# Optimization experiments

Measured on AMD Instinct MI355X. Metric: run time of the kernel, lower is better.

Reference implementation:

```python
import jax, jax.numpy as jnp
import numpy as np

B_, C0, H_, W_ = 2, 64, 128, 128
NB = 4          # number of VSS blocks (depths=[4])
K = 4           # scan directions
DI = 128        # d_inner = 2.0 * 64
N = 16          # ssm_d_state
R = 4           # dt_rank = ceil(64/16)


def setup_inputs() -> dict:
    key = jax.random.key(0)
    ks = jax.random.split(key, 16)
    rn = lambda k, shape, s: jax.random.normal(k, shape, jnp.float32) * s
    inp = {}
    inp["inp_img"] = jax.random.normal(ks[0], (B_, 1, H_, W_), jnp.float32)
    inp["x"] = jax.random.normal(ks[1], (B_, C0, H_, W_), jnp.float32)
    inp["y"] = jax.random.normal(ks[2], (B_, C0, H_, W_), jnp.float32)
    inp["reduce_w"] = rn(ks[3], (64, 128, 1, 1), 0.05)
    inp["patch_w"] = rn(ks[4], (64, 64, 1, 1), 0.05)
    inp["patch_g"] = jnp.ones((64,)); inp["patch_b"] = jnp.zeros((64,))
    inp["ln1_g"] = jnp.ones((NB, 64)); inp["ln1_b"] = jnp.zeros((NB, 64))
    inp["in_proj_w"] = rn(ks[5], (NB, 2 * DI, 64), 0.05)
    inp["conv_w"] = rn(ks[6], (NB, DI, 1, 3, 3), 0.1)   # depthwise 3x3
    inp["conv_b"] = jnp.zeros((NB, DI))
    inp["x_proj_w"] = rn(ks[7], (NB, K, R + 2 * N, DI), 0.05)
    inp["dt_proj_w"] = rn(ks[8], (NB, K, DI, R), 0.1)
    inp["dt_proj_b"] = rn(ks[9], (NB, K, DI), 0.1)
    A = jnp.tile(jnp.arange(1, N + 1, dtype=jnp.float32)[None, :], (K * DI, 1))
    inp["A_logs"] = jnp.tile(jnp.log(A)[None], (NB, 1, 1))
    inp["Ds_p"] = jnp.ones((NB, K * DI))
    inp["out_norm_g"] = jnp.ones((NB, DI)); inp["out_norm_b"] = jnp.zeros((NB, DI))
    inp["out_proj_w"] = rn(ks[10], (NB, 64, DI), 0.05)
    inp["ln2_g"] = jnp.ones((NB, 64)); inp["ln2_b"] = jnp.zeros((NB, 64))
    inp["fc1_w"] = rn(ks[11], (NB, 256, 64), 0.05); inp["fc1_b"] = jnp.zeros((NB, 256))
    inp["fc2_w"] = rn(ks[12], (NB, 64, 256), 0.05); inp["fc2_b"] = jnp.zeros((NB, 64))
    inp["out1_w"] = rn(ks[13], (32, 64, 3, 3), 0.05)
    inp["out2_w"] = rn(ks[14], (1, 32, 3, 3), 0.05)
    return inp


def conv2d(t, w, pad=0, groups=1):
    return jax.lax.conv_general_dilated(
        t, w, (1, 1), [(pad, pad), (pad, pad)],
        dimension_numbers=("NCHW", "OIHW", "NCHW"), feature_group_count=groups)


def ln(t, g, b):
    mu = t.mean(-1, keepdims=True)
    v = t.var(-1, keepdims=True)
    return (t - mu) / jnp.sqrt(v + 1e-5) * g + b


def ssm_scan(u, delta, A, Bs, Cs):
    # u, delta: (B,K,D,L); A: (K,D,N); Bs, Cs: (B,K,N,L)
    Bn = u.shape[0]
    ut = jnp.moveaxis(u, -1, 0)      # (L,B,K,D)
    dt = jnp.moveaxis(delta, -1, 0)
    Bt = jnp.moveaxis(Bs, -1, 0)     # (L,B,K,N)
    Ct = jnp.moveaxis(Cs, -1, 0)
    h0 = jnp.zeros((Bn, K, DI, N), u.dtype)
    def step(h, inp):
        u_, d_, b_, c_ = inp
        h = jnp.exp(d_[..., None] * A) * h + (d_ * u_)[..., None] * b_[:, :, None, :]
        return h, jnp.sum(h * c_[:, :, None, :], -1)
    _, ys = jax.lax.scan(step, h0, (ut, dt, Bt, Ct))
    return jnp.moveaxis(ys, 0, -1)   # (B,K,D,L)


def vss_block(t, i, ln1_g, ln1_b, in_proj_w, conv_w, conv_b, x_proj_w,
              dt_proj_w, dt_proj_b, A_logs, Ds_p, out_norm_g, out_norm_b,
              out_proj_w, ln2_g, ln2_b, fc1_w, fc1_b, fc2_w, fc2_b):
    # t: (B,H,W,64)
    h = ln(t, ln1_g[i], ln1_b[i])
    xz = jnp.einsum("bhwc,oc->bhwo", h, in_proj_w[i])     # (B,H,W,2*DI)
    xp, zp = jnp.split(xz, 2, axis=-1)
    xc = jnp.transpose(xp, (0, 3, 1, 2))                    # (B,DI,H,W)
    xc = conv2d(xc, conv_w[i], pad=1, groups=DI) + conv_b[i][None, :, None, None]
    xc = jax.nn.silu(xc)
    Bn, D, H, W = xc.shape
    L = H * W
    x_hw = xc.reshape(Bn, D, L)
    x_wh = jnp.transpose(xc, (0, 1, 3, 2)).reshape(Bn, D, L)
    xs = jnp.stack([x_hw, x_wh, jnp.flip(x_hw, -1), jnp.flip(x_wh, -1)], 1)  # (B,K,D,L)
    x_dbl = jnp.einsum("bkdl,kcd->bkcl", xs, x_proj_w[i])
    dts, Bs, Cs = jnp.split(x_dbl, [R, R + N], axis=2)
    dts = jnp.einsum("bkrl,kdr->bkdl", dts, dt_proj_w[i])
    delta = jax.nn.softplus(dts + dt_proj_b[i][None, :, :, None])
    A = -jnp.exp(A_logs[i]).reshape(K, D, N)
    ys = ssm_scan(xs, delta, A, Bs, Cs)
    ys = ys + Ds_p[i].reshape(K, D)[None, :, :, None] * xs
    # cross-merge
    ym = ys[:, 0] + jnp.flip(ys[:, 2], -1)
    ywh = ys[:, 1] + jnp.flip(ys[:, 3], -1)
    ym = ym + jnp.transpose(ywh.reshape(Bn, D, W, H), (0, 1, 3, 2)).reshape(Bn, D, L)
    yo = jnp.transpose(ym.reshape(Bn, D, H, W), (0, 2, 3, 1))  # (B,H,W,DI)
    yo = ln(yo, out_norm_g[i], out_norm_b[i])
    yo = yo * jax.nn.silu(zp)
    t = t + jnp.einsum("bhwd,od->bhwo", yo, out_proj_w[i])
    m = ln(t, ln2_g[i], ln2_b[i])
    m = jax.nn.gelu(jnp.einsum("bhwc,oc->bhwo", m, fc1_w[i]) + fc1_b[i], approximate=False)
    m = jnp.einsum("bhwc,oc->bhwo", m, fc2_w[i]) + fc2_b[i]
    return t + m


def reference(inp_img, x, y, reduce_w, patch_w, patch_g, patch_b, ln1_g, ln1_b,
              in_proj_w, conv_w, conv_b, x_proj_w, dt_proj_w, dt_proj_b, A_logs,
              Ds_p, out_norm_g, out_norm_b, out_proj_w, ln2_g, ln2_b, fc1_w,
              fc1_b, fc2_w, fc2_b, out1_w, out2_w):
    f = conv2d(jnp.concatenate([x, y], 1), reduce_w)          # (B,64,H,W)
    t = jnp.transpose(conv2d(f, patch_w), (0, 2, 3, 1))        # (B,H,W,64)
    t = ln(t, patch_g, patch_b)
    for i in range(NB):
        t = vss_block(t, i, ln1_g, ln1_b, in_proj_w, conv_w, conv_b, x_proj_w,
                      dt_proj_w, dt_proj_b, A_logs, Ds_p, out_norm_g, out_norm_b,
                      out_proj_w, ln2_g, ln2_b, fc1_w, fc1_b, fc2_w, fc2_b)
    z = jnp.transpose(t, (0, 3, 1, 2))                         # (B,64,H,W)
    o = conv2d(z, out1_w, pad=1)
    o = jnp.where(o >= 0, o, 0.01 * o)                         # LeakyReLU
    o = conv2d(o, out2_w, pad=1) + inp_img
    return jax.nn.sigmoid(o), f
```

## Files before the change

kernel.cpp:

```cpp
#include <hip/hip_runtime.h>
#include <math.h>

#define B_ 2
#define H_ 128
#define W_ 128
#define L_ (H_*W_)
#define DI 128
#define NK 4
#define NST 16
#define NBLK 4
#define C36 36

__device__ __forceinline__ int scan_src(int k, int l){
  if (k == 0)      return l;
  else if (k == 1) return ((l & 127) << 7) | (l >> 7);
  else if (k == 2) return L_-1-l;
  else { int m = L_-1-l; return ((m & 127) << 7) | (m >> 7); }
}

template<int NCHT>
__device__ __forceinline__ void scan_decode(int g, int& b, int& k, int& c){
  int xcd = g & 7, s = g >> 3;
  int m = s & 1, qh = s >> 1;
  int q = qh*8 + xcd;
  b = q / (2*NCHT);
  int rc = (q / NCHT) & 1;
  int cc = q % NCHT;
  k = rc ? (m ? 3 : 1) : (m ? 2 : 0);
  c = m ? (NCHT-1-cc) : cc;
}

__global__ void k_repack(const float* __restrict__ inw, const float* __restrict__ f1w,
                         const float* __restrict__ f2w, const float* __restrict__ opw,
                         const float* __restrict__ redw, const float* __restrict__ patw,
                         const float* __restrict__ o1w, const float* __restrict__ o2w,
                         const float* __restrict__ xpjw, float* __restrict__ wr){
  int idx = blockIdx.x*256 + threadIdx.x;
  if (idx >= 358688) return;
  float v;
  if (idx < 65536){
    int i = idx >> 14, r = idx & 16383; int k = r >> 8, o = r & 255;
    v = inw[(size_t)(i*256 + o)*64 + k];
  } else if (idx < 131072){
    int j = idx - 65536; int i = j >> 14, r = j & 16383; int k = r >> 8, o = r & 255;
    v = f1w[(size_t)(i*256 + o)*64 + k];
  } else if (idx < 196608){
    int j = idx - 131072; int i = j >> 14, r = j & 16383; int k = r >> 6, o = r & 63;
    v = f2w[(size_t)(i*64 + o)*256 + k];
  } else if (idx < 229376){
    int j = idx - 196608; int i = j >> 13, r = j & 8191; int k = r >> 6, o = r & 63;
    v = opw[(size_t)(i*64 + o)*128 + k];
  } else if (idx < 237568){
    int j = idx - 229376; int k = j >> 6, o = j & 63;
    v = redw[o*128 + k];
  } else if (idx < 241664){
    int j = idx - 237568; int k = j >> 6, o = j & 63;
    v = patw[o*64 + k];
  } else if (idx < 260096){
    int j = idx - 241664; int tap = j >> 11, r = j & 2047; int k = r >> 5, o = r & 31;
    v = o1w[(size_t)(o*64 + k)*9 + tap];
  } else if (idx < 260384){
    int j = idx - 260096; int tap = j >> 5, c = j & 31;
    v = o2w[c*9 + tap];
  } else {
    int j = idx - 260384;
    int grp = j / 1536, r3 = j % 1536;
    int d = r3 / 12, jj = r3 % 12;
    int cg = grp & 3; int ik = grp >> 2;
    v = (jj < 9) ? xpjw[((size_t)(ik*36) + cg*9 + jj)*128 + d] : 0.f;
  }
  wr[idx] = v;
}

__global__ __launch_bounds__(256) void k_reduce(
    const float* __restrict__ x, const float* __restrict__ y,
    const float* __restrict__ w, float* __restrict__ f){
  __shared__ float Xs[128*68];
  int tid = threadIdx.x;
  int blk = blockIdx.x; int b = blk >> 8; int l0 = (blk & 255)*64;
  const float* xb = x + (size_t)b*64*L_ + l0;
  const float* yb = y + (size_t)b*64*L_ + l0;
  #pragma unroll
  for (int rep = 0; rep < 32; ++rep){
    int idx = rep*256 + tid;
    int k = idx >> 6, p = idx & 63;
    float v = (k < 64) ? xb[(size_t)k*L_ + p] : yb[(size_t)(k-64)*L_ + p];
    Xs[k*68 + p] = v;
  }
  __syncthreads();
  int p0 = (tid & 15)*4, o0 = (tid >> 4)*4;
  float acc[4][4] = {};
  #pragma unroll 2
  for (int k = 0; k < 128; ++k){
    float4 xa = *(const float4*)&Xs[k*68 + p0];
    float4 wa = *(const float4*)&w[k*64 + o0];
    float xv[4] = {xa.x,xa.y,xa.z,xa.w};
    float wv[4] = {wa.x,wa.y,wa.z,wa.w};
    #pragma unroll
    for (int a = 0; a < 4; ++a)
      #pragma unroll
      for (int o = 0; o < 4; ++o) acc[a][o] += xv[a]*wv[o];
  }
  #pragma unroll
  for (int o = 0; o < 4; ++o){
    float* dst = f + (size_t)(b*64 + o0 + o)*L_ + l0 + p0;
    *(float4*)dst = make_float4(acc[0][o],acc[1][o],acc[2][o],acc[3][o]);
  }
}

__global__ __launch_bounds__(256) void k_patch_ln(
    const float* __restrict__ f, const float* __restrict__ w,
    const float* __restrict__ pg, const float* __restrict__ pb,
    float* __restrict__ t){
  __shared__ float Xs[64*68];
  __shared__ float Os[64*65];
  __shared__ float stat[128];
  int tid = threadIdx.x;
  int blk = blockIdx.x; int b = blk >> 8; int l0 = (blk & 255)*64;
  const float* fb = f + (size_t)b*64*L_ + l0;
  #pragma unroll
  for (int rep = 0; rep < 16; ++rep){
    int idx = rep*256 + tid;
    int k = idx >> 6, p = idx & 63;
    Xs[k*68 + p] = fb[(size_t)k*L_ + p];
  }
  __syncthreads();
  int p0 = (tid & 15)*4, o0 = (tid >> 4)*4;
  float acc[4][4] = {};
  #pragma unroll 2
  for (int k = 0; k < 64; ++k){
    float4 xa = *(const float4*)&Xs[k*68 + p0];
    float4 wa = *(const float4*)&w[k*64 + o0];
    float xv[4] = {xa.x,xa.y,xa.z,xa.w};
    float wv[4] = {wa.x,wa.y,wa.z,wa.w};
    #pragma unroll
    for (int a = 0; a < 4; ++a)
      #pragma unroll
      for (int o = 0; o < 4; ++o) acc[a][o] += xv[a]*wv[o];
  }
  #pragma unroll
  for (int a = 0; a < 4; ++a)
    #pragma unroll
    for (int o = 0; o < 4; ++o)
      Os[(p0+a)*65 + o0+o] = acc[a][o];
  __syncthreads();
  if (tid < 64){
    float s = 0.f, s2 = 0.f;
    #pragma unroll
    for (int c = 0; c < 64; ++c){ float v = Os[tid*65+c]; s += v; s2 += v*v; }
    float mu = s*(1.f/64), var = s2*(1.f/64) - mu*mu;
    stat[tid*2] = mu; stat[tid*2+1] = rsqrtf(var + 1e-5f);
  }
  __syncthreads();
  #pragma unroll
  for (int rep = 0; rep < 16; ++rep){
    int idx = rep*256 + tid;
    int p = idx >> 6, c = idx & 63;
    float mu = stat[p*2], rstd = stat[p*2+1];
    t[(size_t)blk*64*64 + idx] = (Os[p*65+c]-mu)*rstd*pg[c] + pb[c];
  }
}

__global__ __launch_bounds__(256) void k_ln_inproj(
    const float* __restrict__ t, const float* __restrict__ g,
    const float* __restrict__ bta, const float* __restrict__ w,
    float* __restrict__ xp, float* __restrict__ zt){
  __shared__ float raw[64*65];
  __shared__ float Xs[64*68];
  __shared__ float scr[512];
  __shared__ float stat[128];
  int tid = threadIdx.x;
  int pix0 = blockIdx.x*64;
  const float* tb = t + (size_t)pix0*64;
  #pragma unroll
  for (int rep = 0; rep < 16; ++rep){
    int idx = rep*256 + tid;
    int p = idx >> 6, c = idx & 63;
    raw[p*65 + c] = tb[idx];
  }
  __syncthreads();
  int p = tid & 63, q = tid >> 6;
  {
    float s = 0.f, s2 = 0.f;
    #pragma unroll
    for (int i = 0; i < 16; ++i){ float v = raw[p*65 + q*16 + i]; s += v; s2 += v*v; }
    scr[p*8 + q*2] = s; scr[p*8 + q*2 + 1] = s2;
  }
  __syncthreads();
  if (tid < 64){
    float s = 0.f, s2 = 0.f;
    #pragma unroll
    for (int j = 0; j < 4; ++j){ s += scr[tid*8 + j*2]; s2 += scr[tid*8 + j*2 + 1]; }
    float mu = s*(1.f/64), var = s2*(1.f/64) - mu*mu;
    stat[tid] = mu; stat[64+tid] = rsqrtf(var + 1e-5f);
  }
  __syncthreads();
  {
    float mu = stat[p], rstd = stat[64+p];
    #pragma unroll
    for (int i = 0; i < 16; ++i){
      int c = q*16 + i;
      Xs[c*68 + p] = (raw[p*65+c] - mu)*rstd*g[c] + bta[c];
    }
  }
  __syncthreads();
  int p0 = (tid & 7)*8, o0 = (tid >> 3)*8;
  float acc[8][8] = {};
  #pragma unroll 2
  for (int k = 0; k < 64; ++k){
    float4 xa = *(const float4*)&Xs[k*68 + p0];
    float4 xb = *(const float4*)&Xs[k*68 + p0 + 4];
    float4 wa = *(const float4*)&w[k*256 + o0];
    float4 wb = *(const float4*)&w[k*256 + o0 + 4];
    float xv[8] = {xa.x,xa.y,xa.z,xa.w,xb.x,xb.y,xb.z,xb.w};
    float wv[8] = {wa.x,wa.y,wa.z,wa.w,wb.x,wb.y,wb.z,wb.w};
    #pragma unroll
    for (int a = 0; a < 8; ++a)
      #pragma unroll
      for (int o = 0; o < 8; ++o) acc[a][o] += xv[a]*wv[o];
  }
  if (o0 < 128){
    float* base = xp + (size_t)pix0*128 + o0;
    #pragma unroll
    for (int a = 0; a < 8; ++a){
      float* dst = base + (size_t)(p0+a)*128;
      *(float4*)dst     = make_float4(acc[a][0],acc[a][1],acc[a][2],acc[a][3]);
      *(float4*)(dst+4) = make_float4(acc[a][4],acc[a][5],acc[a][6],acc[a][7]);
    }
  } else {
    int oz = o0 - 128;
    float* dstz = zt + (size_t)blockIdx.x*8192;
    #pragma unroll
    for (int o = 0; o < 8; ++o){
      *(float4*)&dstz[(oz+o)*64 + p0]     = make_float4(acc[0][o],acc[1][o],acc[2][o],acc[3][o]);
      *(float4*)&dstz[(oz+o)*64 + p0 + 4] = make_float4(acc[4][o],acc[5][o],acc[6][o],acc[7][o]);
    }
  }
}

__global__ __launch_bounds__(256) void k_dwconv(
    const float* __restrict__ xp, const float* __restrict__ cw,
    const float* __restrict__ cb, float* __restrict__ xc){
  int idx = blockIdx.x*256 + threadIdx.x;
  int d = idx & 127; int tt = idx >> 7;
  int w = tt & 127; tt >>= 7;
  int h0 = (tt & 31)*4; int b = tt >> 5;
  float wt[9];
  #pragma unroll
  for (int q = 0; q < 9; ++q) wt[q] = cw[d*9+q];
  float cbv = cb[d];
  float acc[4] = {cbv, cbv, cbv, cbv};
  const float* base = xp + (size_t)(b*L_)*128 + d;
  #pragma unroll
  for (int r = 0; r < 6; ++r){
    int rr = h0 - 1 + r;
    if ((unsigned)rr >= 128u) continue;
    const float* rowp = base + (size_t)(rr*128 + w)*128;
    float mid   = rowp[0];
    float left  = (w > 0)   ? rowp[-128] : 0.f;
    float right = (w < 127) ? rowp[128]  : 0.f;
    #pragma unroll
    for (int i = 0; i < 4; ++i){
      int kh = rr - (h0 + i) + 1;
      if (0 <= kh && kh <= 2)
        acc[i] += left*wt[kh*3] + mid*wt[kh*3+1] + right*wt[kh*3+2];
    }
  }
  #pragma unroll
  for (int i = 0; i < 4; ++i){
    float a = acc[i];
    xc[((size_t)(b*L_ + (h0+i)*128 + w))*128 + d] = a/(1.f + __expf(-a));
  }
}

__global__ __launch_bounds__(256) void k_xproj(
    const float* __restrict__ xc, const float* __restrict__ wxp,
    float* __restrict__ xdbl){
  int lt = blockIdx.x & 255; int bk = blockIdx.x >> 8;
  int b = bk >> 2, k = bk & 3;
  int l0 = lt*64;
  __shared__ float Ws[4*128*12];
  __shared__ float Xs[64*129];
  int tid = threadIdx.x;
  const float* wsrc = wxp + (size_t)k*6144;
  for (int j = tid; j < 6144; j += 256) Ws[j] = wsrc[j];
  for (int j = tid; j < 64*128; j += 256){
    int lr = j >> 7, d = j & 127;
    Xs[lr*129 + d] = xc[((size_t)(b*L_ + l0 + lr))*128 + d];
  }
  __syncthreads();
  int lx = tid & 63, cg = tid >> 6;
  float acc[9];
  #pragma unroll
  for (int j = 0; j < 9; ++j) acc[j] = 0.f;
  const float* xrow = Xs + lx*129;
  const float* wbase = Ws + cg*128*12;
  #pragma unroll 4
  for (int d = 0; d < 128; ++d){
    float xv = xrow[d];
    const float* wd = wbase + d*12;
    float4 wa = *(const float4*)wd;
    float4 wb = *(const float4*)(wd+4);
    float w8 = wd[8];
    acc[0]+=xv*wa.x; acc[1]+=xv*wa.y; acc[2]+=xv*wa.z; acc[3]+=xv*wa.w;
    acc[4]+=xv*wb.x; acc[5]+=xv*wb.y; acc[6]+=xv*wb.z; acc[7]+=xv*wb.w;
    acc[8]+=xv*w8;
  }
  float* out = xdbl + ((size_t)bk*L_ + l0 + lx)*C36 + cg*9;
  #pragma unroll
  for (int j = 0; j < 9; ++j) out[j] = acc[j];
}

template<int PASS, int NCHT, int LCT>
__global__ __launch_bounds__(128, 2) void k_scan_chunk(
    const float* __restrict__ xc, const float* __restrict__ xdbl,
    const float* __restrict__ dtw, const float* __restrict__ dtb,
    const float* __restrict__ ds,
    float* __restrict__ chS, float* __restrict__ chH,
    float* __restrict__ ym){
  __shared__ float rowS[LCT*36];
  int b, k, c;
  scan_decode<NCHT>(blockIdx.x, b, k, c);
  int bk = b*4 + k;
  int blk = bk*NCHT + c;
  int tid = threadIdx.x;
  int d = tid;
  const float* xdb = xdbl + (size_t)bk*L_*C36;
  const int F4 = (PASS == 0) ? 5 : 9;
  for (int idx = tid; idx < LCT*F4; idx += 128){
    int r = idx / F4, f4 = idx - r*F4;
    int src = scan_src(k, c*LCT + r);
    *(float4*)&rowS[r*36 + f4*4] = *(const float4*)(xdb + (size_t)src*C36 + f4*4);
  }
  float4 wv4 = *(const float4*)(dtw + (size_t)(k*128+d)*4);
  float w0 = wv4.x, w1 = wv4.y, w2 = wv4.z, w3 = wv4.w;
  float bb = dtb[k*128+d];
  float Dsv = ds[k*128+d];
  float h[16];
  float S = 0.f;
  size_t chbase = ((size_t)blk*128 + d)*16;
  if (PASS == 0){
    #pragma unroll
    for (int n = 0; n < 16; ++n) h[n] = 0.f;
  } else {
    #pragma unroll
    for (int qq = 0; qq < 4; ++qq){
      float4 v = *(const float4*)(chH + chbase + qq*4);
      h[qq*4+0]=v.x; h[qq*4+1]=v.y; h[qq*4+2]=v.z; h[qq*4+3]=v.w;
    }
  }
  int sbase = scan_src(k, c*LCT);
  int sstep = (k == 0) ? 1 : (k == 1) ? 128 : (k == 2) ? -1 : -128;
  ptrdiff_t stepOff = (ptrdiff_t)sstep*128;
  const float* up = xc + (size_t)b*L_*128 + (size_t)sbase*128 + d;
  float* yp = ym + (size_t)b*L_*128 + (size_t)sbase*128 + d;
  __syncthreads();
  float u = *up;
  #pragma unroll 2
  for (int j = 0; j < LCT; ++j){
    up += stepOff;
    float u_nxt = *up;
    const float* r = rowS + j*36;
    float4 dtv = *(const float4*)r;
    float xdt = bb + dtv.x*w0 + dtv.y*w1 + dtv.z*w2 + dtv.w*w3;
    float ex = __expf(xdt);
    float delta = (xdt > 20.f) ? xdt : __logf(1.f + ex);
    float e1 = __builtin_amdgcn_rcpf(1.f + ex);
    float e2 = e1*e1, e3 = e2*e1, e4 = e2*e2;
    float e8 = e4*e4, e12 = e8*e4;
    float mm[16];
    mm[0]=e1;      mm[1]=e2;      mm[2]=e3;      mm[3]=e4;
    mm[4]=e4*e1;   mm[5]=e4*e2;   mm[6]=e4*e3;   mm[7]=e8;
    mm[8]=e8*e1;   mm[9]=e8*e2;   mm[10]=e8*e3;  mm[11]=e8*e4;
    mm[12]=e12*e1; mm[13]=e12*e2; mm[14]=e12*e3; mm[15]=e12*e4;
    float du = delta * u;
    if (PASS == 0){
      S += delta;
      #pragma unroll
      for (int qq = 0; qq < 4; ++qq){
        float4 Bq = *(const float4*)(r + 4 + qq*4);
        h[qq*4+0] = mm[qq*4+0]*h[qq*4+0] + du*Bq.x;
        h[qq*4+1] = mm[qq*4+1]*h[qq*4+1] + du*Bq.y;
        h[qq*4+2] = mm[qq*4+2]*h[qq*4+2] + du*Bq.z;
        h[qq*4+3] = mm[qq*4+3]*h[qq*4+3] + du*Bq.w;
      }
    } else {
      float y = Dsv * u;
      #pragma unroll
      for (int qq = 0; qq < 4; ++qq){
        float4 Bq = *(const float4*)(r + 4 + qq*4);
        float4 Cq = *(const float4*)(r + 20 + qq*4);
        h[qq*4+0] = mm[qq*4+0]*h[qq*4+0] + du*Bq.x;  y += h[qq*4+0]*Cq.x;
        h[qq*4+1] = mm[qq*4+1]*h[qq*4+1] + du*Bq.y;  y += h[qq*4+1]*Cq.y;
        h[qq*4+2] = mm[qq*4+2]*h[qq*4+2] + du*Bq.z;  y += h[qq*4+2]*Cq.z;
        h[qq*4+3] = mm[qq*4+3]*h[qq*4+3] + du*Bq.w;  y += h[qq*4+3]*Cq.w;
      }
      atomicAdd(yp, y);
      yp += stepOff;
    }
    u = u_nxt;
  }
  if (PASS == 0){
    #pragma unroll
    for (int qq = 0; qq < 4; ++qq)
      *(float4*)(chH + chbase + qq*4) =
        make_float4(h[qq*4+0],h[qq*4+1],h[qq*4+2],h[qq*4+3]);
    chS[blk*128 + d] = S;
  }
}

template<int NCHT>
__global__ __launch_bounds__(256) void k_scan_fix(
    const float* __restrict__ chS, float* __restrict__ chH,
    float* __restrict__ ym){
  int blk = blockIdx.x;
  if (blk >= 32){
    float4 z4 = make_float4(0.f,0.f,0.f,0.f);
    float4* dst = (float4*)ym + (size_t)(blk-32)*512 + threadIdx.x;
    dst[0]   = z4;
    dst[256] = z4;
    return;
  }
  if (threadIdx.x >= 128) return;
  int bk = blk >> 2; int nq = blk & 3;
  int d = threadIdx.x;
  float4 h = make_float4(0.f, 0.f, 0.f, 0.f);
  float  Sr[8]; float4 Hr[8];
  #pragma unroll
  for (int i = 0; i < 8; ++i){
    int cb = bk*NCHT + i;
    Sr[i] = chS[cb*128 + d];
    Hr[i] = *(const float4*)(chH + ((size_t)cb*128 + d)*16 + nq*4);
  }
  for (int c4 = 0; c4 < NCHT; c4 += 8){
    float  Sn[8]; float4 Hn[8];
    #pragma unroll
    for (int i = 0; i < 8; ++i){
      int cc = c4 + 8 + i; if (cc > NCHT-1) cc = NCHT-1;
      int cb = bk*NCHT + cc;
      Sn[i] = chS[cb*128 + d];
      Hn[i] = *(const float4*)(chH + ((size_t)cb*128 + d)*16 + nq*4);
    }
    #pragma unroll
    for (int i = 0; i < 8; ++i){
      int cb = bk*NCHT + c4 + i;
      size_t base = ((size_t)cb*128 + d)*16 + nq*4;
      float S = Sr[i]; float4 Hf = Hr[i];
      *(float4*)(chH + base) = h;
      float eS = __expf(-S);
      float e2 = eS*eS, e4 = e2*e2, e8 = e4*e4;
      float ep;
      if (nq == 0) ep = eS;
      else if (nq == 1) ep = e4*eS;
      else if (nq == 2) ep = e8*eS;
      else ep = e8*e4*eS;
      h.x = ep*h.x + Hf.x; ep *= eS;
      h.y = ep*h.y + Hf.y; ep *= eS;
      h.z = ep*h.z + Hf.z; ep *= eS;
      h.w = ep*h.w + Hf.w;
    }
    #pragma unroll
    for (int i = 0; i < 8; ++i){ Sr[i] = Sn[i]; Hr[i] = Hn[i]; }
  }
}

__global__ __launch_bounds__(512) void k_gate_mlp(
    const float* __restrict__ ym, const float* __restrict__ zt,
    const float* __restrict__ ong, const float* __restrict__ onb,
    const float* __restrict__ wop,
    const float* __restrict__ g2, const float* __restrict__ bt2,
    const float* __restrict__ w1, const float* __restrict__ b1,
    const float* __restrict__ w2, const float* __restrict__ b2,
    float* __restrict__ t){
  __shared__ float raw[64*65];
  __shared__ float ymYs[128*68];
  __shared__ float Xs[64*68];
  __shared__ float stat[128];
  __shared__ float scr[64*17];
  int tid = threadIdx.x;
  int tile = blockIdx.x;
  int pix0 = tile*64;
  #pragma unroll
  for (int rep = 0; rep < 8; ++rep){
    int idx = rep*512 + tid; int p = idx >> 6, c = idx & 63;
    raw[p*65 + c] = t[(size_t)pix0*64 + idx];
  }
  #pragma unroll
  for (int rep = 0; rep < 16; ++rep){
    int idx = rep*512 + tid; int p = idx >> 7, c = idx & 127;
    ymYs[c*68 + p] = ym[(size_t)pix0*128 + idx];
  }
  __syncthreads();
  int p = tid & 63, q = tid >> 6;
  int qq = __builtin_amdgcn_readfirstlane(q);
  {
    float s = 0.f, s2 = 0.f;
    #pragma unroll
    for (int i = 0; i < 16; ++i){ float v = ymYs[(q*16+i)*68 + p]; s += v; s2 += v*v; }
    scr[p*17 + q*2] = s; scr[p*17 + q*2 + 1] = s2;
  }
  __syncthreads();
  if (tid < 64){
    float s = 0.f, s2 = 0.f;
    #pragma unroll
    for (int j = 0; j < 8; ++j){ s += scr[tid*17 + j*2]; s2 += scr[tid*17 + j*2 + 1]; }
    float mu = s*(1.f/128), var = s2*(1.f/128) - mu*mu;
    stat[tid] = mu; stat[64+tid] = rsqrtf(var + 1e-5f);
  }
  __syncthreads();
  {
    float mu = stat[p], rstd = stat[64+p];
    const float* ztb = zt + (size_t)tile*8192;
    #pragma unroll 4
    for (int i = 0; i < 16; ++i){
      int c = q*16 + i;
      float zv = ztb[c*64 + p];
      float yo = (ymYs[c*68+p]-mu)*rstd*ong[c] + onb[c];
      ymYs[c*68+p] = yo * zv / (1.f + __expf(-zv));
    }
  }
  __syncthreads();
  int o0 = qq*8;
  {
    float acc[8] = {};
    const float* wb = wop + o0;
    #pragma unroll 4
    for (int k = 0; k < 128; ++k){
      float xa = ymYs[k*68 + p];
      float4 wa = *(const float4*)&wb[k*64];
      float4 wc = *(const float4*)&wb[k*64 + 4];
      acc[0] += xa*wa.x; acc[1] += xa*wa.y; acc[2] += xa*wa.z; acc[3] += xa*wa.w;
      acc[4] += xa*wc.x; acc[5] += xa*wc.y; acc[6] += xa*wc.z; acc[7] += xa*wc.w;
    }
    #pragma unroll
    for (int o = 0; o < 8; ++o)
      raw[p*65 + o0 + o] += acc[o];
  }
  __syncthreads();
  {
    float s = 0.f, s2 = 0.f;
    #pragma unroll
    for (int i = 0; i < 8; ++i){ float v = raw[p*65 + q*8 + i]; s += v; s2 += v*v; }
    scr[p*17 + q*2] = s; scr[p*17 + q*2 + 1] = s2;
  }
  __syncthreads();
  if (tid < 64){
    float s = 0.f, s2 = 0.f;
    #pragma unroll
    for (int j = 0; j < 8; ++j){ s += scr[tid*17 + j*2]; s2 += scr[tid*17 + j*2 + 1]; }
    float mu = s*(1.f/64), var = s2*(1.f/64) - mu*mu;
    stat[tid] = mu; stat[64+tid] = rsqrtf(var + 1e-5f);
  }
  __syncthreads();
  {
    float mu = stat[p], rstd = stat[64+p];
    #pragma unroll
    for (int i = 0; i < 8; ++i){
      int c = q*8 + i;
      Xs[c*68 + p] = (raw[p*65+c]-mu)*rstd*g2[c] + bt2[c];
    }
  }
  __syncthreads();
  float acc2[8] = {};
  int o1 = qq*16;
  #pragma unroll
  for (int ch = 0; ch < 2; ++ch){
    float acc1[16] = {};
    {
      const float* wb = w1 + ch*128 + o1;
      #pragma unroll 4
      for (int k = 0; k < 64; ++k){
        float xa = Xs[k*68 + p];
        float4 wa = *(const float4*)&wb[k*256];
        float4 wc = *(const float4*)&wb[k*256 + 4];
        float4 we = *(const float4*)&wb[k*256 + 8];
        float4 wg = *(const float4*)&wb[k*256 + 12];
        acc1[0]  += xa*wa.x; acc1[1]  += xa*wa.y; acc1[2]  += xa*wa.z; acc1[3]  += xa*wa.w;
        acc1[4]  += xa*wc.x; acc1[5]  += xa*wc.y; acc1[6]  += xa*wc.z; acc1[7]  += xa*wc.w;
        acc1[8]  += xa*we.x; acc1[9]  += xa*we.y; acc1[10] += xa*we.z; acc1[11] += xa*we.w;
        acc1[12] += xa*wg.x; acc1[13] += xa*wg.y; acc1[14] += xa*wg.z; acc1[15] += xa*wg.w;
      }
    }
    __syncthreads();
    {
      #pragma unroll
      for (int o = 0; o < 16; ++o){
        float v = acc1[o] + b1[ch*128 + o1 + o];
        ymYs[(o1+o)*68 + p] = 0.5f*v*(1.f + erff(v*0.70710678118654752f));
      }
    }
    __syncthreads();
    {
      const float* wb = w2 + (size_t)(ch*128)*64 + o0;
      #pragma unroll 4
      for (int kk = 0; kk < 128; ++kk){
        float xa = ymYs[kk*68 + p];
        float4 wa = *(const float4*)&wb[kk*64];
        float4 wc = *(const float4*)&wb[kk*64 + 4];
        acc2[0] += xa*wa.x; acc2[1] += xa*wa.y; acc2[2] += xa*wa.z; acc2[3] += xa*wa.w;
        acc2[4] += xa*wc.x; acc2[5] += xa*wc.y; acc2[6] += xa*wc.z; acc2[7] += xa*wc.w;
      }
    }
  }
  {
    float4 ba = *(const float4*)&b2[o0];
    float4 bc = *(const float4*)&b2[o0 + 4];
    float4 o4a, o4b;
    o4a.x = raw[p*65 + o0    ] + acc2[0] + ba.x;
    o4a.y = raw[p*65 + o0 + 1] + acc2[1] + ba.y;
    o4a.z = raw[p*65 + o0 + 2] + acc2[2] + ba.z;
    o4a.w = raw[p*65 + o0 + 3] + acc2[3] + ba.w;
    o4b.x = raw[p*65 + o0 + 4] + acc2[4] + bc.x;
    o4b.y = raw[p*65 + o0 + 5] + acc2[5] + bc.y;
    o4b.z = raw[p*65 + o0 + 6] + acc2[6] + bc.z;
    o4b.w = raw[p*65 + o0 + 7] + acc2[7] + bc.w;
    float* dst = &t[(size_t)(pix0+p)*64 + o0];
    *(float4*)dst     = o4a;
    *(float4*)(dst+4) = o4b;
  }
}

__global__ __launch_bounds__(256) void k_out1(
    const float* __restrict__ t, const float* __restrict__ w,
    float* __restrict__ o1){
  __shared__ float tS[64*136];
  int tid = threadIdx.x;
  int blk = blockIdx.x;
  int b = blk >> 8; int rem = blk & 255;
  int h0 = (rem >> 2)*2, w0 = (rem & 3)*32;
  #pragma unroll
  for (int rep = 0; rep < 34; ++rep){
    int idx = rep*256 + tid;
    int gidx = idx >> 6, c = idx & 63;
    int row = gidx / 34, col = gidx % 34;
    int hh = h0 - 1 + row, ww = w0 - 1 + col;
    float v = 0.f;
    if ((unsigned)hh < 128u && (unsigned)ww < 128u)
      v = t[(size_t)(b*L_ + hh*128 + ww)*64 + c];
    tS[c*136 + gidx] = v;
  }
  __syncthreads();
  int oj = tid & 7;
  int pix = tid >> 3;
  int r = pix >> 4, cc = pix & 15;
  float acc[2][4] = {};
  #pragma unroll
  for (int tap = 0; tap < 9; ++tap){
    int dr = tap/3, dc = tap%3;
    int g1 = (r + dr)*34 + cc + dc;
    const float* wt = w + (size_t)tap*64*32 + 4*oj;
    #pragma unroll 4
    for (int k = 0; k < 64; ++k){
      float xv1 = tS[k*136 + g1];
      float xv2 = tS[k*136 + g1 + 16];
      float4 wv = *(const float4*)&wt[k*32];
      acc[0][0] += xv1*wv.x; acc[0][1] += xv1*wv.y; acc[0][2] += xv1*wv.z; acc[0][3] += xv1*wv.w;
      acc[1][0] += xv2*wv.x; acc[1][1] += xv2*wv.y; acc[1][2] += xv2*wv.z; acc[1][3] += xv2*wv.w;
    }
  }
  #pragma unroll
  for (int pp = 0; pp < 2; ++pp){
    int h = h0 + r, wv_ = w0 + cc + pp*16;
    float* dst = o1 + (size_t)(b*L_ + h*128 + wv_)*32 + 4*oj;
    float4 o4;
    o4.x = acc[pp][0] >= 0.f ? acc[pp][0] : 0.01f*acc[pp][0];
    o4.y = acc[pp][1] >= 0.f ? acc[pp][1] : 0.01f*acc[pp][1];
    o4.z = acc[pp][2] >= 0.f ? acc[pp][2] : 0.01f*acc[pp][2];
    o4.w = acc[pp][3] >= 0.f ? acc[pp][3] : 0.01f*acc[pp][3];
    *(float4*)dst = o4;
  }
}

__global__ __launch_bounds__(256) void k_out2(
    const float* __restrict__ o1, const float* __restrict__ w,
    const float* __restrict__ img, float* __restrict__ out){
  __shared__ float oS[32*401];
  int tid = threadIdx.x;
  int blk = blockIdx.x;
  int b = blk >> 6; int rem = blk & 63;
  int h0 = (rem >> 1)*4, w0 = (rem & 1)*64;
  for (int idx = tid; idx < 396*32; idx += 256){
    int gidx = idx >> 5, c = idx & 31;
    int row = gidx / 66, col = gidx % 66;
    int hh = h0 - 1 + row, ww = w0 - 1 + col;
    float v = 0.f;
    if ((unsigned)hh < 128u && (unsigned)ww < 128u)
      v = o1[(size_t)(b*L_ + hh*128 + ww)*32 + c];
    oS[c*401 + gidx] = v;
  }
  __syncthreads();
  int row = tid >> 6, ww = tid & 63;
  float acc = 0.f;
  #pragma unroll
  for (int tap = 0; tap < 9; ++tap){
    int dr = tap/3, dc = tap%3;
    int g = (row + dr)*66 + ww + dc;
    #pragma unroll 8
    for (int k = 0; k < 32; ++k)
      acc += oS[k*401 + g] * w[tap*32 + k];
  }
  int oi = b*L_ + (h0+row)*128 + w0 + ww;
  acc += img[oi];
  out[oi] = 1.f/(1.f + __expf(-acc));
}

extern "C" void kernel_launch(void* const* d_in, const int* in_sizes, int n_in,
                              void* d_out, int out_size, void* d_ws, size_t ws_size,
                              hipStream_t stream){
  const float* inp_img   = (const float*)d_in[0];
  const float* x         = (const float*)d_in[1];
  const float* y         = (const float*)d_in[2];
  const float* reduce_w  = (const float*)d_in[3];
  const float* patch_w   = (const float*)d_in[4];
  const float* patch_g   = (const float*)d_in[5];
  const float* patch_b   = (const float*)d_in[6];
  const float* ln1_g     = (const float*)d_in[7];
  const float* ln1_b     = (const float*)d_in[8];
  const float* in_proj_w = (const float*)d_in[9];
  const float* conv_w    = (const float*)d_in[10];
  const float* conv_b    = (const float*)d_in[11];
  const float* x_proj_w  = (const float*)d_in[12];
  const float* dt_proj_w = (const float*)d_in[13];
  const float* dt_proj_b = (const float*)d_in[14];
  const float* Ds_p      = (const float*)d_in[16];
  const float* out_norm_g= (const float*)d_in[17];
  const float* out_norm_b= (const float*)d_in[18];
  const float* out_proj_w= (const float*)d_in[19];
  const float* ln2_g     = (const float*)d_in[20];
  const float* ln2_b     = (const float*)d_in[21];
  const float* fc1_w     = (const float*)d_in[22];
  const float* fc1_b     = (const float*)d_in[23];
  const float* fc2_w     = (const float*)d_in[24];
  const float* fc2_b     = (const float*)d_in[25];
  const float* out1_w    = (const float*)d_in[26];
  const float* out2_w    = (const float*)d_in[27];

  float* out_sig = (float*)d_out;
  float* f       = (float*)d_out + (size_t)B_*L_;

  float* ws   = (float*)d_ws;
  float* t    = ws;
  float* xp   = t    + (size_t)B_*L_*64;
  float* zt   = xp   + (size_t)B_*L_*128;
  float* xc   = zt   + (size_t)B_*L_*128;
  float* xdbl = xc   + (size_t)B_*L_*128;
  float* ym   = xdbl + (size_t)B_*NK*L_*C36;
  float* wr   = ym   + (size_t)B_*L_*128;
  float* chS  = wr   + 358688;
  float* chH = xp;
  float* o1  = ym;

  bool big = ws_size >= (size_t)24213792 * sizeof(float);

  float* wr_in  = wr;
  float* wr_f1  = wr + 65536;
  float* wr_f2  = wr + 131072;
  float* wr_op  = wr + 196608;
  float* wr_red = wr + 229376;
  float* wr_pat = wr + 237568;
  float* wr_o1  = wr + 241664;
  float* wr_o2  = wr + 260096;
  float* wr_xp  = wr + 260384;

  k_repack<<<1402, 256, 0, stream>>>(in_proj_w, fc1_w, fc2_w, out_proj_w,
                                     reduce_w, patch_w, out1_w, out2_w, x_proj_w, wr);
  k_reduce<<<512, 256, 0, stream>>>(x, y, wr_red, f);
  k_patch_ln<<<512, 256, 0, stream>>>(f, wr_pat, patch_g, patch_b, t);
  for (int i = 0; i < NBLK; ++i){
    k_ln_inproj<<<512, 256, 0, stream>>>(t, ln1_g + i*64, ln1_b + i*64,
                                         wr_in + (size_t)i*16384, xp, zt);
    k_dwconv<<<4096, 256, 0, stream>>>(xp, conv_w + i*128*9, conv_b + i*128, xc);
    k_xproj<<<2048, 256, 0, stream>>>(xc, wr_xp + (size_t)i*24576, xdbl);
    if (big){
      k_scan_chunk<0,256,64><<<B_*NK*256, 128, 0, stream>>>(
          xc, xdbl, dt_proj_w + i*NK*128*4, dt_proj_b + i*NK*128,
          Ds_p + i*NK*128, chS, chH, ym);
      k_scan_fix<256><<<2080, 256, 0, stream>>>(chS, chH, ym);
      k_scan_chunk<1,256,64><<<B_*NK*256, 128, 0, stream>>>(
          xc, xdbl, dt_proj_w + i*NK*128*4, dt_proj_b + i*NK*128,
          Ds_p + i*NK*128, chS, chH, ym);
    } else {
      k_scan_chunk<0,128,128><<<B_*NK*128, 128, 0, stream>>>(
          xc, xdbl, dt_proj_w + i*NK*128*4, dt_proj_b + i*NK*128,
          Ds_p + i*NK*128, chS, chH, ym);
      k_scan_fix<128><<<2080, 256, 0, stream>>>(chS, chH, ym);
      k_scan_chunk<1,128,128><<<B_*NK*128, 128, 0, stream>>>(
          xc, xdbl, dt_proj_w + i*NK*128*4, dt_proj_b + i*NK*128,
          Ds_p + i*NK*128, chS, chH, ym);
    }
    k_gate_mlp<<<512, 512, 0, stream>>>(ym, zt, out_norm_g + i*128, out_norm_b + i*128,
                                        wr_op + (size_t)i*8192,
                                        ln2_g + i*64, ln2_b + i*64,
                                        wr_f1 + (size_t)i*16384, fc1_b + i*256,
                                        wr_f2 + (size_t)i*16384, fc2_b + i*64, t);
  }
  k_out1<<<512, 256, 0, stream>>>(t, wr_o1, o1);
  k_out2<<<128, 256, 0, stream>>>(o1, wr_o2, inp_img, out_sig);
}
```

Baseline: 1.278 ms.

## Process two channels per thread in scan chunks with 64-thread blocks

The chunked selective-scan kernel now runs one wavefront of 64 threads per block, and each thread handles two d_inner channels (d and d+64). The B values from shared memory are loaded once and reused for both channels, which halves the per-row LDS traffic and gives each thread two independent recurrences for more instruction-level parallelism. The fix kernel is re-split so that each block handles 64 channels, and its grid grows to match. The cost is roughly double the register pressure per thread (two 16-float states) and fewer threads per block, which may lower occupancy or cause spilling.

```diff
diff --git a/kernel.cpp b/kernel.cpp
--- a/kernel.cpp
+++ b/kernel.cpp
@@ -312,7 +312,7 @@
 }
 
 template<int PASS, int NCHT, int LCT>
-__global__ __launch_bounds__(128, 2) void k_scan_chunk(
+__global__ __launch_bounds__(64) void k_scan_chunk(
     const float* __restrict__ xc, const float* __restrict__ xdbl,
     const float* __restrict__ dtw, const float* __restrict__ dtb,
     const float* __restrict__ ds,
@@ -324,88 +324,125 @@
   int bk = b*4 + k;
   int blk = bk*NCHT + c;
   int tid = threadIdx.x;
-  int d = tid;
+  int dA = tid, dB = tid + 64;
   const float* xdb = xdbl + (size_t)bk*L_*C36;
   const int F4 = (PASS == 0) ? 5 : 9;
-  for (int idx = tid; idx < LCT*F4; idx += 128){
+  for (int idx = tid; idx < LCT*F4; idx += 64){
     int r = idx / F4, f4 = idx - r*F4;
     int src = scan_src(k, c*LCT + r);
     *(float4*)&rowS[r*36 + f4*4] = *(const float4*)(xdb + (size_t)src*C36 + f4*4);
   }
-  float4 wv4 = *(const float4*)(dtw + (size_t)(k*128+d)*4);
-  float w0 = wv4.x, w1 = wv4.y, w2 = wv4.z, w3 = wv4.w;
-  float bb = dtb[k*128+d];
-  float Dsv = ds[k*128+d];
-  float h[16];
-  float S = 0.f;
-  size_t chbase = ((size_t)blk*128 + d)*16;
+  float4 wvA = *(const float4*)(dtw + (size_t)(k*128+dA)*4);
+  float4 wvB = *(const float4*)(dtw + (size_t)(k*128+dB)*4);
+  float bbA = dtb[k*128+dA], bbB = dtb[k*128+dB];
+  float DsA = ds[k*128+dA],  DsB = ds[k*128+dB];
+  float hA[16], hB[16];
+  float SA = 0.f, SB = 0.f;
+  size_t chbA = ((size_t)blk*128 + dA)*16;
+  size_t chbB = ((size_t)blk*128 + dB)*16;
   if (PASS == 0){
     #pragma unroll
-    for (int n = 0; n < 16; ++n) h[n] = 0.f;
+    for (int n = 0; n < 16; ++n){ hA[n] = 0.f; hB[n] = 0.f; }
   } else {
     #pragma unroll
     for (int qq = 0; qq < 4; ++qq){
-      float4 v = *(const float4*)(chH + chbase + qq*4);
-      h[qq*4+0]=v.x; h[qq*4+1]=v.y; h[qq*4+2]=v.z; h[qq*4+3]=v.w;
+      float4 vA = *(const float4*)(chH + chbA + qq*4);
+      float4 vB = *(const float4*)(chH + chbB + qq*4);
+      hA[qq*4+0]=vA.x; hA[qq*4+1]=vA.y; hA[qq*4+2]=vA.z; hA[qq*4+3]=vA.w;
+      hB[qq*4+0]=vB.x; hB[qq*4+1]=vB.y; hB[qq*4+2]=vB.z; hB[qq*4+3]=vB.w;
     }
   }
   int sbase = scan_src(k, c*LCT);
   int sstep = (k == 0) ? 1 : (k == 1) ? 128 : (k == 2) ? -1 : -128;
   ptrdiff_t stepOff = (ptrdiff_t)sstep*128;
-  const float* up = xc + (size_t)b*L_*128 + (size_t)sbase*128 + d;
-  float* yp = ym + (size_t)b*L_*128 + (size_t)sbase*128 + d;
-  __syncthreads();
-  float u = *up;
-  #pragma unroll 2
+  const float* up = xc + (size_t)b*L_*128 + (size_t)sbase*128 + dA;
+  float* yp = ym + (size_t)b*L_*128 + (size_t)sbase*128 + dA;
+  __syncthreads();
+  float uA = up[0], uB = up[64];
   for (int j = 0; j < LCT; ++j){
     up += stepOff;
-    float u_nxt = *up;
+    float uA_n = up[0], uB_n = up[64];
     const float* r = rowS + j*36;
     float4 dtv = *(const float4*)r;
-    float xdt = bb + dtv.x*w0 + dtv.y*w1 + dtv.z*w2 + dtv.w*w3;
-    float ex = __expf(xdt);
-    float delta = (xdt > 20.f) ? xdt : __logf(1.f + ex);
-    float e1 = __builtin_amdgcn_rcpf(1.f + ex);
-    float e2 = e1*e1, e3 = e2*e1, e4 = e2*e2;
-    float e8 = e4*e4, e12 = e8*e4;
-    float mm[16];
-    mm[0]=e1;      mm[1]=e2;      mm[2]=e3;      mm[3]=e4;
-    mm[4]=e4*e1;   mm[5]=e4*e2;   mm[6]=e4*e3;   mm[7]=e8;
-    mm[8]=e8*e1;   mm[9]=e8*e2;   mm[10]=e8*e3;  mm[11]=e8*e4;
-    mm[12]=e12*e1; mm[13]=e12*e2; mm[14]=e12*e3; mm[15]=e12*e4;
-    float du = delta * u;
-    if (PASS == 0){
-      S += delta;
-      #pragma unroll
-      for (int qq = 0; qq < 4; ++qq){
-        float4 Bq = *(const float4*)(r + 4 + qq*4);
-        h[qq*4+0] = mm[qq*4+0]*h[qq*4+0] + du*Bq.x;
-        h[qq*4+1] = mm[qq*4+1]*h[qq*4+1] + du*Bq.y;
-        h[qq*4+2] = mm[qq*4+2]*h[qq*4+2] + du*Bq.z;
-        h[qq*4+3] = mm[qq*4+3]*h[qq*4+3] + du*Bq.w;
+    float4 Bq0 = *(const float4*)(r + 4);
+    float4 Bq1 = *(const float4*)(r + 8);
+    float4 Bq2 = *(const float4*)(r + 12);
+    float4 Bq3 = *(const float4*)(r + 16);
+    float Bn[16] = {Bq0.x,Bq0.y,Bq0.z,Bq0.w, Bq1.x,Bq1.y,Bq1.z,Bq1.w,
+                    Bq2.x,Bq2.y,Bq2.z,Bq2.w, Bq3.x,Bq3.y,Bq3.z,Bq3.w};
+    {
+      float xdt = bbA + dtv.x*wvA.x + dtv.y*wvA.y + dtv.z*wvA.z + dtv.w*wvA.w;
+      float ex = __expf(xdt);
+      float delta = (xdt > 20.f) ? xdt : __logf(1.f + ex);
+      float e1 = __builtin_amdgcn_rcpf(1.f + ex);
+      float e2 = e1*e1, e3 = e2*e1, e4 = e2*e2;
+      float e8 = e4*e4, e12 = e8*e4;
+      float mm[16];
+      mm[0]=e1;      mm[1]=e2;      mm[2]=e3;      mm[3]=e4;
+      mm[4]=e4*e1;   mm[5]=e4*e2;   mm[6]=e4*e3;   mm[7]=e8;
+      mm[8]=e8*e1;   mm[9]=e8*e2;   mm[10]=e8*e3;  mm[11]=e8*e4;
+      mm[12]=e12*e1; mm[13]=e12*e2; mm[14]=e12*e3; mm[15]=e12*e4;
+      float du = delta * uA;
+      if (PASS == 0){
+        SA += delta;
+        #pragma unroll
+        for (int n = 0; n < 16; ++n) hA[n] = mm[n]*hA[n] + du*Bn[n];
+      } else {
+        float y = DsA * uA;
+        #pragma unroll
+        for (int qq = 0; qq < 4; ++qq){
+          float4 Cq = *(const float4*)(r + 20 + qq*4);
+          hA[qq*4+0] = mm[qq*4+0]*hA[qq*4+0] + du*Bn[qq*4+0];  y += hA[qq*4+0]*Cq.x;
+          hA[qq*4+1] = mm[qq*4+1]*hA[qq*4+1] + du*Bn[qq*4+1];  y += hA[qq*4+1]*Cq.y;
+          hA[qq*4+2] = mm[qq*4+2]*hA[qq*4+2] + du*Bn[qq*4+2];  y += hA[qq*4+2]*Cq.z;
+          hA[qq*4+3] = mm[qq*4+3]*hA[qq*4+3] + du*Bn[qq*4+3];  y += hA[qq*4+3]*Cq.w;
+        }
+        atomicAdd(yp, y);
       }
-    } else {
-      float y = Dsv * u;
-      #pragma unroll
-      for (int qq = 0; qq < 4; ++qq){
-        float4 Bq = *(const float4*)(r + 4 + qq*4);
-        float4 Cq = *(const float4*)(r + 20 + qq*4);
-        h[qq*4+0] = mm[qq*4+0]*h[qq*4+0] + du*Bq.x;  y += h[qq*4+0]*Cq.x;
-        h[qq*4+1] = mm[qq*4+1]*h[qq*4+1] + du*Bq.y;  y += h[qq*4+1]*Cq.y;
-        h[qq*4+2] = mm[qq*4+2]*h[qq*4+2] + du*Bq.z;  y += h[qq*4+2]*Cq.z;
-        h[qq*4+3] = mm[qq*4+3]*h[qq*4+3] + du*Bq.w;  y += h[qq*4+3]*Cq.w;
+    }
+    {
+      float xdt = bbB + dtv.x*wvB.x + dtv.y*wvB.y + dtv.z*wvB.z + dtv.w*wvB.w;
+      float ex = __expf(xdt);
+      float delta = (xdt > 20.f) ? xdt : __logf(1.f + ex);
+      float e1 = __builtin_amdgcn_rcpf(1.f + ex);
+      float e2 = e1*e1, e3 = e2*e1, e4 = e2*e2;
+      float e8 = e4*e4, e12 = e8*e4;
+      float mm[16];
+      mm[0]=e1;      mm[1]=e2;      mm[2]=e3;      mm[3]=e4;
+      mm[4]=e4*e1;   mm[5]=e4*e2;   mm[6]=e4*e3;   mm[7]=e8;
+      mm[8]=e8*e1;   mm[9]=e8*e2;   mm[10]=e8*e3;  mm[11]=e8*e4;
+      mm[12]=e12*e1; mm[13]=e12*e2; mm[14]=e12*e3; mm[15]=e12*e4;
+      float du = delta * uB;
+      if (PASS == 0){
+        SB += delta;
+        #pragma unroll
+        for (int n = 0; n < 16; ++n) hB[n] = mm[n]*hB[n] + du*Bn[n];
+      } else {
+        float y = DsB * uB;
+        #pragma unroll
+        for (int qq = 0; qq < 4; ++qq){
+          float4 Cq = *(const float4*)(r + 20 + qq*4);
+          hB[qq*4+0] = mm[qq*4+0]*hB[qq*4+0] + du*Bn[qq*4+0];  y += hB[qq*4+0]*Cq.x;
+          hB[qq*4+1] = mm[qq*4+1]*hB[qq*4+1] + du*Bn[qq*4+1];  y += hB[qq*4+1]*Cq.y;
+          hB[qq*4+2] = mm[qq*4+2]*hB[qq*4+2] + du*Bn[qq*4+2];  y += hB[qq*4+2]*Cq.z;
+          hB[qq*4+3] = mm[qq*4+3]*hB[qq*4+3] + du*Bn[qq*4+3];  y += hB[qq*4+3]*Cq.w;
+        }
+        atomicAdd(yp + 64, y);
+        yp += stepOff;
       }
-      atomicAdd(yp, y);
-      yp += stepOff;
-    }
-    u = u_nxt;
+    }
+    uA = uA_n; uB = uB_n;
   }
   if (PASS == 0){
     #pragma unroll
-    for (int qq = 0; qq < 4; ++qq)
-      *(float4*)(chH + chbase + qq*4) =
-        make_float4(h[qq*4+0],h[qq*4+1],h[qq*4+2],h[qq*4+3]);
-    chS[blk*128 + d] = S;
+    for (int qq = 0; qq < 4; ++qq){
+      *(float4*)(chH + chbA + qq*4) =
+        make_float4(hA[qq*4+0],hA[qq*4+1],hA[qq*4+2],hA[qq*4+3]);
+      *(float4*)(chH + chbB + qq*4) =
+        make_float4(hB[qq*4+0],hB[qq*4+1],hB[qq*4+2],hB[qq*4+3]);
+    }
+    chS[blk*128 + dA] = SA;
+    chS[blk*128 + dB] = SB;
   }
 }
 
@@ -414,16 +451,17 @@
     const float* __restrict__ chS, float* __restrict__ chH,
     float* __restrict__ ym){
   int blk = blockIdx.x;
-  if (blk >= 32){
+  if (blk >= 64){
     float4 z4 = make_float4(0.f,0.f,0.f,0.f);
-    float4* dst = (float4*)ym + (size_t)(blk-32)*512 + threadIdx.x;
+    float4* dst = (float4*)ym + (size_t)(blk-64)*512 + threadIdx.x;
     dst[0]   = z4;
     dst[256] = z4;
     return;
   }
-  if (threadIdx.x >= 128) return;
-  int bk = blk >> 2; int nq = blk & 3;
-  int d = threadIdx.x;
+  if (threadIdx.x >= 64) return;
+  int bknq = blk >> 1, dh = blk & 1;
+  int bk = bknq >> 2; int nq = bknq & 3;
+  int d = dh*64 + threadIdx.x;
   float4 h = make_float4(0.f, 0.f, 0.f, 0.f);
   float  Sr[8]; float4 Hr[8];
   #pragma unroll
@@ -772,19 +810,19 @@
     k_dwconv<<<4096, 256, 0, stream>>>(xp, conv_w + i*128*9, conv_b + i*128, xc);
     k_xproj<<<2048, 256, 0, stream>>>(xc, wr_xp + (size_t)i*24576, xdbl);
     if (big){
-      k_scan_chunk<0,256,64><<<B_*NK*256, 128, 0, stream>>>(
+      k_scan_chunk<0,256,64><<<B_*NK*256, 64, 0, stream>>>(
           xc, xdbl, dt_proj_w + i*NK*128*4, dt_proj_b + i*NK*128,
           Ds_p + i*NK*128, chS, chH, ym);
-      k_scan_fix<256><<<2080, 256, 0, stream>>>(chS, chH, ym);
-      k_scan_chunk<1,256,64><<<B_*NK*256, 128, 0, stream>>>(
+      k_scan_fix<256><<<2112, 256, 0, stream>>>(chS, chH, ym);
+      k_scan_chunk<1,256,64><<<B_*NK*256, 64, 0, stream>>>(
           xc, xdbl, dt_proj_w + i*NK*128*4, dt_proj_b + i*NK*128,
           Ds_p + i*NK*128, chS, chH, ym);
     } else {
-      k_scan_chunk<0,128,128><<<B_*NK*128, 128, 0, stream>>>(
+      k_scan_chunk<0,128,128><<<B_*NK*128, 64, 0, stream>>>(
           xc, xdbl, dt_proj_w + i*NK*128*4, dt_proj_b + i*NK*128,
           Ds_p + i*NK*128, chS, chH, ym);
-      k_scan_fix<128><<<2080, 256, 0, stream>>>(chS, chH, ym);
-      k_scan_chunk<1,128,128><<<B_*NK*128, 128, 0, stream>>>(
+      k_scan_fix<128><<<2112, 256, 0, stream>>>(chS, chH, ym);
+      k_scan_chunk<1,128,128><<<B_*NK*128, 64, 0, stream>>>(
           xc, xdbl, dt_proj_w + i*NK*128*4, dt_proj_b + i*NK*128,
           Ds_p + i*NK*128, chS, chH, ym);
     }
```

New measurement: 1.351 ms. 1.06x slower.
